# Kernel optimization log

Measured on AMD Instinct MI355X. Metric: run time of the kernel, lower is better.

## Reference

```python
import jax, jax.numpy as jnp
import numpy as np

B, T, DH, DS, A = 32, 2048, 1024, 1024, 512

def setup_inputs() -> dict:
    key = jax.random.key(0)
    k1, k2, k3, k4, k5 = jax.random.split(key, 5)
    s = jax.random.normal(k1, (B, DS), dtype=jnp.float32)
    h = jax.random.normal(k2, (B, T, DH), dtype=jnp.float32)
    # glorot_uniform for W_a, U_a; uniform(-0.05, 0.05) for v_a (Keras defaults)
    lim_W = np.sqrt(6.0 / (DS + A)).astype(np.float32)
    lim_U = np.sqrt(6.0 / (DH + A)).astype(np.float32)
    W_a = jax.random.uniform(k3, (DS, A), minval=-lim_W, maxval=lim_W, dtype=jnp.float32)
    U_a = jax.random.uniform(k4, (DH, A), minval=-lim_U, maxval=lim_U, dtype=jnp.float32)
    v_a = jax.random.uniform(k5, (A,), minval=-0.05, maxval=0.05, dtype=jnp.float32)
    return {"s": s, "h": h, "W_a": W_a, "U_a": U_a, "v_a": v_a}

def reference(s, h, W_a, U_a, v_a):
    # U_a_h: [B, T, A]; W_a_s: [B, 1, A]
    U_a_h = jnp.einsum('btd,da->bta', h, U_a)
    W_a_s = (s @ W_a)[:, None, :]
    e = jnp.tanh(W_a_s + U_a_h)          # [B, T, A]
    e = jnp.einsum('bta,a->bt', e, v_a)   # learned-vector reduction
    a = jax.nn.softmax(e, axis=-1)        # exp / sum over time (same math, stable)
    c = jnp.einsum('bt,btd->bd', a, h)    # weighted sum over time
    return c
```

## Files before the change

kernel.cpp:

```cpp
#include <hip/hip_runtime.h>
#include <hip/hip_bf16.h>

#define B_  32
#define T_  2048
#define DH_ 1024
#define DS_ 1024
#define A_  512
#define M_  (B_ * T_)

typedef __attribute__((ext_vector_type(8))) short bf16x8;
typedef __attribute__((ext_vector_type(4))) float f32x4;

__device__ __forceinline__ unsigned short f2bf(float f) {
    union { float f; unsigned u; } v; v.f = f;
    unsigned r = 0x7FFFu + ((v.u >> 16) & 1u);
    return (unsigned short)((v.u + r) >> 16);
}
__device__ __forceinline__ float fast_tanh(float x) {
    float cx = fminf(fmaxf(x, -9.f), 9.f);
    float e2 = __expf(2.f * cx);
    return (e2 - 1.f) / (e2 + 1.f);
}
__device__ __forceinline__ unsigned pack_bf2(float lo, float hi) {
    union { float f; unsigned u; } a, b;
    a.f = lo; b.f = hi;
    return __builtin_amdgcn_perm(b.u + 0x8000u, a.u + 0x8000u, 0x07060302u);
}

__global__ void prep_ut(const float* __restrict__ U, unsigned short* __restrict__ Ut) {
    int o = blockIdx.x * 256 + threadIdx.x;
    int a = o >> 10, k = o & (DH_ - 1);
    Ut[o] = f2bf(U[k * A_ + a]);
}

__global__ void ws_gemv2(const float* __restrict__ s, const float* __restrict__ W,
                         float* __restrict__ Ws) {
    __shared__ float red[4][64];
    const int blk = blockIdx.x;
    const int b = blk >> 3, a0 = (blk & 7) * 64;
    const int tid = threadIdx.x;
    const int a = a0 + (tid & 63), kq = tid >> 6;
    const float* sp = s + b * DS_ + kq * 256;
    const float* wp = W + (size_t)(kq * 256) * A_ + a;
    float acc = 0.f;
#pragma unroll 8
    for (int k = 0; k < 256; ++k) acc += sp[k] * wp[(size_t)k * A_];
    red[kq][tid & 63] = acc;
    __syncthreads();
    if (tid < 64)
        Ws[b * A_ + a0 + tid] = red[0][tid] + red[1][tid] + red[2][tid] + red[3][tid];
}

__global__ void __launch_bounds__(512, 2)
gemm_bn512(const float* __restrict__ h,
           const unsigned short* __restrict__ Ut,
           const float* __restrict__ Ws, const float* __restrict__ va,
           float* __restrict__ e) {
    __shared__ unsigned short As[2][128][32];
    __shared__ unsigned short Bs[2][512][32];

    const int tid = threadIdx.x;
    const int tm = blockIdx.x;
    const int rowBase = tm * 128;

    const int lane = tid & 63;
    const int wid = tid >> 6;
    const int wm = wid >> 2, wn = wid & 3;
    const int lr = lane & 15, kg = lane >> 4;
    const int gsw16 = (kg ^ ((lr >> 1) & 3)) * 8;

    const int ar = tid >> 2;
    const int alg = tid & 3;

    f32x4 acc[4][8];
#pragma unroll
    for (int i = 0; i < 4; ++i)
#pragma unroll
        for (int j = 0; j < 8; ++j) acc[i][j] = (f32x4){0.f, 0.f, 0.f, 0.f};

    auto loadA = [&](float4* areg, int t) {
        const float* hp = h + (size_t)(rowBase + ar) * DH_ + t * 32 + alg * 8;
        areg[0] = *(const float4*)(hp);
        areg[1] = *(const float4*)(hp + 4);
    };
    auto stageB = [&](int buf, int t) {
        const int k0 = t * 32;
#pragma unroll
        for (int j = 0; j < 4; ++j) {
            int byt = j * 8192 + tid * 16;
            int r = byt >> 6;
            int g = ((byt >> 4) & 3) ^ ((r >> 1) & 3);
            const unsigned short* gb = Ut + (size_t)r * DH_ + k0 + g * 8;
            __builtin_amdgcn_global_load_lds(
                (const __attribute__((address_space(1))) unsigned int*)gb,
                (__attribute__((address_space(3))) unsigned int*)(&Bs[buf][0][0] + (byt >> 1)),
                16, 0, 0);
        }
    };
    auto packwriteA = [&](const float4* areg, int buf) {
        uint4 u;
        u.x = pack_bf2(areg[0].x, areg[0].y);
        u.y = pack_bf2(areg[0].z, areg[0].w);
        u.z = pack_bf2(areg[1].x, areg[1].y);
        u.w = pack_bf2(areg[1].z, areg[1].w);
        int p = alg ^ ((ar >> 1) & 3);
        *(uint4*)((char*)&As[buf][0][0] + ar * 64 + p * 16) = u;
    };

    float4 areg[2];
    const int NT = DH_ / 32;

    loadA(areg, 0);
    __builtin_amdgcn_sched_barrier(0);
    stageB(0, 0);
    __builtin_amdgcn_sched_barrier(0);
    packwriteA(areg, 0);
    asm volatile("s_waitcnt vmcnt(0) lgkmcnt(0)" ::: "memory");
    __builtin_amdgcn_s_barrier();
    __builtin_amdgcn_sched_barrier(0);

#pragma unroll 1
    for (int t = 0; t < NT; ++t) {
        const int buf = t & 1;
        const bool more = (t < NT - 1);
        if (more) {
            loadA(areg, t + 1);
            __builtin_amdgcn_sched_barrier(0);
            stageB(buf ^ 1, t + 1);
            __builtin_amdgcn_sched_barrier(0);
        }

        const unsigned short* Ab = &As[buf][0][0];
        const unsigned short* Bb = &Bs[buf][0][0];
        bf16x8 af[4], bq[8];
#pragma unroll
        for (int nf = 0; nf < 8; ++nf)
            bq[nf] = *(const bf16x8*)(Bb + (wn * 128 + nf * 16 + lr) * 32 + gsw16);
#pragma unroll
        for (int mi = 0; mi < 4; ++mi)
            af[mi] = *(const bf16x8*)(Ab + (wm * 64 + mi * 16 + lr) * 32 + gsw16);
        asm volatile("s_waitcnt lgkmcnt(0)" ::: "memory");
        __builtin_amdgcn_sched_barrier(0);

        __builtin_amdgcn_s_setprio(1);
#pragma unroll
        for (int mi = 0; mi < 4; ++mi)
#pragma unroll
            for (int nf = 0; nf < 8; ++nf)
                acc[mi][nf] = __builtin_amdgcn_mfma_f32_16x16x32_bf16(
                    af[mi], bq[nf], acc[mi][nf], 0, 0, 0);
        __builtin_amdgcn_s_setprio(0);
        __builtin_amdgcn_sched_barrier(0);

        if (more) {
            packwriteA(areg, buf ^ 1);
            asm volatile("s_waitcnt vmcnt(0) lgkmcnt(0)" ::: "memory");
            __builtin_amdgcn_s_barrier();
            __builtin_amdgcn_sched_barrier(0);
        }
    }
    __syncthreads();

    const int bIdx = rowBase >> 11;
    const float* WsRow = Ws + bIdx * A_;
    float wsv[8], vav[8];
#pragma unroll
    for (int nf = 0; nf < 8; ++nf) {
        int a = wn * 128 + nf * 16 + lr;
        wsv[nf] = WsRow[a];
        vav[nf] = va[a];
    }
    float* pf = (float*)&As[0][0][0];
#pragma unroll
    for (int mi = 0; mi < 4; ++mi) {
#pragma unroll
        for (int j = 0; j < 4; ++j) {
            float ssum = 0.f;
#pragma unroll
            for (int nf = 0; nf < 8; ++nf) {
                float x = acc[mi][nf][j] + wsv[nf];
                ssum += fast_tanh(x) * vav[nf];
            }
            ssum += __shfl_xor(ssum, 1);
            ssum += __shfl_xor(ssum, 2);
            ssum += __shfl_xor(ssum, 4);
            ssum += __shfl_xor(ssum, 8);
            if (lr == 0) {
                int r = wm * 64 + mi * 16 + kg * 4 + j;
                pf[r * 4 + wn] = ssum;
            }
        }
    }
    __syncthreads();
    if (tid < 128) {
        float v0 = pf[tid * 4 + 0] + pf[tid * 4 + 1] + pf[tid * 4 + 2] + pf[tid * 4 + 3];
        e[rowBase + tid] = v0;
    }
}

__global__ void smax_ctx(const float* __restrict__ e, const float* __restrict__ h,
                         float* __restrict__ c) {
    __shared__ float al[T_];
    __shared__ float red[8];
    __shared__ float part[256];
    const int b = blockIdx.x >> 3, dseg = blockIdx.x & 7;
    const int tid = threadIdx.x;
    const float* ep = e + (size_t)b * T_;

    float4 v0 = ((const float4*)ep)[tid * 2];
    float4 v1 = ((const float4*)ep)[tid * 2 + 1];
    float m = fmaxf(fmaxf(fmaxf(v0.x, v0.y), fmaxf(v0.z, v0.w)),
                    fmaxf(fmaxf(v1.x, v1.y), fmaxf(v1.z, v1.w)));
#pragma unroll
    for (int off = 1; off < 64; off <<= 1) m = fmaxf(m, __shfl_xor(m, off));
    const int wv = tid >> 6;
    if ((tid & 63) == 0) red[wv] = m;
    __syncthreads();
    m = fmaxf(fmaxf(red[0], red[1]), fmaxf(red[2], red[3]));
    float e0 = __expf(v0.x - m), e1 = __expf(v0.y - m);
    float e2 = __expf(v0.z - m), e3 = __expf(v0.w - m);
    float e4 = __expf(v1.x - m), e5 = __expf(v1.y - m);
    float e6 = __expf(v1.z - m), e7 = __expf(v1.w - m);
    float ssum = e0 + e1 + e2 + e3 + e4 + e5 + e6 + e7;
#pragma unroll
    for (int off = 1; off < 64; off <<= 1) ssum += __shfl_xor(ssum, off);
    if ((tid & 63) == 0) red[4 + wv] = ssum;
    al[tid * 8 + 0] = e0; al[tid * 8 + 1] = e1;
    al[tid * 8 + 2] = e2; al[tid * 8 + 3] = e3;
    al[tid * 8 + 4] = e4; al[tid * 8 + 5] = e5;
    al[tid * 8 + 6] = e6; al[tid * 8 + 7] = e7;
    __syncthreads();
    const float inv = 1.f / (red[4] + red[5] + red[6] + red[7]);

    const int d = dseg * 128 + (tid & 127);
    const int th = tid >> 7;
    const float* hp = h + ((size_t)b * T_ + th) * DH_ + d;
    float acc = 0.f;
#pragma unroll 8
    for (int t = 0; t < T_ / 2; ++t)
        acc += al[2 * t + th] * hp[(size_t)(2 * t) * DH_];
    part[tid] = acc;
    __syncthreads();
    if (tid < 128)
        c[(size_t)b * DH_ + dseg * 128 + tid] = (part[tid] + part[tid + 128]) * inv;
}

extern "C" void kernel_launch(void* const* d_in, const int* in_sizes, int n_in,
                              void* d_out, int out_size, void* d_ws, size_t ws_size,
                              hipStream_t stream) {
    const float* s   = (const float*)d_in[0];
    const float* h   = (const float*)d_in[1];
    const float* W_a = (const float*)d_in[2];
    const float* U_a = (const float*)d_in[3];
    const float* v_a = (const float*)d_in[4];
    float* c = (float*)d_out;

    float* e  = (float*)d_ws;
    float* Ws = e + M_;
    unsigned short* Ut = (unsigned short*)(Ws + B_ * A_);

    prep_ut<<<(A_ * DH_) / 256, 256, 0, stream>>>(U_a, Ut);
    ws_gemv2<<<B_ * 8, 256, 0, stream>>>(s, W_a, Ws);
    gemm_bn512<<<M_ / 128, 512, 0, stream>>>(h, Ut, Ws, v_a, e);
    smax_ctx<<<B_ * 8, 256, 0, stream>>>(e, h, c);
}
```

Baseline: 205.0 us.

## Fuse softmax and context sum into GEMM epilogue with split-T chunk combine

The score GEMM kernel now also computes, for each 128-row time chunk, a local max, the exp weights and their sum, then re-reads the chunk's h rows (likely still in L2) to form a partial context vector. A small combine kernel rescales the 16 chunk partials per batch into the final output, flash-attention style. This removes the separate softmax/context kernel's second full pass over h from HBM. The cost is a serialized tree reduction with many barriers in the epilogue and extra partial-context traffic. The NCH=16 constant assumes 128-row tiles over T=2048.

```diff
diff --git a/kernel.cpp b/kernel.cpp
--- a/kernel.cpp
+++ b/kernel.cpp
@@ -7,6 +7,7 @@
 #define DS_ 1024
 #define A_  512
 #define M_  (B_ * T_)
+#define NCH 16
 
 typedef __attribute__((ext_vector_type(8))) short bf16x8;
 typedef __attribute__((ext_vector_type(4))) float f32x4;
@@ -52,10 +53,11 @@
 }
 
 __global__ void __launch_bounds__(512, 2)
-gemm_bn512(const float* __restrict__ h,
-           const unsigned short* __restrict__ Ut,
-           const float* __restrict__ Ws, const float* __restrict__ va,
-           float* __restrict__ e) {
+fused_chunk(const float* __restrict__ h,
+            const unsigned short* __restrict__ Ut,
+            const float* __restrict__ Ws, const float* __restrict__ va,
+            float* __restrict__ pm, float* __restrict__ pl,
+            float* __restrict__ pc) {
     __shared__ unsigned short As[2][128][32];
     __shared__ unsigned short Bs[2][512][32];
 
@@ -161,6 +163,11 @@
     }
     __syncthreads();
 
+    float* er_s  = (float*)&As[0][0][0];
+    float* red_s = er_s + 128;
+    float* w_s   = er_s + 256;
+    float* pf    = er_s + 384;
+
     const int bIdx = rowBase >> 11;
     const float* WsRow = Ws + bIdx * A_;
     float wsv[8], vav[8];
@@ -170,7 +177,6 @@
         wsv[nf] = WsRow[a];
         vav[nf] = va[a];
     }
-    float* pf = (float*)&As[0][0][0];
 #pragma unroll
     for (int mi = 0; mi < 4; ++mi) {
 #pragma unroll
@@ -193,56 +199,87 @@
     }
     __syncthreads();
     if (tid < 128) {
-        float v0 = pf[tid * 4 + 0] + pf[tid * 4 + 1] + pf[tid * 4 + 2] + pf[tid * 4 + 3];
-        e[rowBase + tid] = v0;
-    }
-}
-
-__global__ void smax_ctx(const float* __restrict__ e, const float* __restrict__ h,
-                         float* __restrict__ c) {
-    __shared__ float al[T_];
-    __shared__ float red[8];
-    __shared__ float part[256];
-    const int b = blockIdx.x >> 3, dseg = blockIdx.x & 7;
+        float v = pf[tid * 4] + pf[tid * 4 + 1] + pf[tid * 4 + 2] + pf[tid * 4 + 3];
+        er_s[tid] = v;
+        red_s[tid] = v;
+    }
+    __syncthreads();
+    if (tid < 64) red_s[tid] = fmaxf(red_s[tid], red_s[tid + 64]);
+    __syncthreads();
+    if (tid < 32) red_s[tid] = fmaxf(red_s[tid], red_s[tid + 32]);
+    __syncthreads();
+    if (tid < 16) red_s[tid] = fmaxf(red_s[tid], red_s[tid + 16]);
+    __syncthreads();
+    if (tid < 8) red_s[tid] = fmaxf(red_s[tid], red_s[tid + 8]);
+    __syncthreads();
+    if (tid < 4) red_s[tid] = fmaxf(red_s[tid], red_s[tid + 4]);
+    __syncthreads();
+    if (tid < 2) red_s[tid] = fmaxf(red_s[tid], red_s[tid + 2]);
+    __syncthreads();
+    if (tid == 0) red_s[0] = fmaxf(red_s[0], red_s[1]);
+    __syncthreads();
+    const float mloc = red_s[0];
+    __syncthreads();
+    if (tid < 128) {
+        float w = __expf(er_s[tid] - mloc);
+        w_s[tid] = w;
+        red_s[tid] = w;
+    }
+    __syncthreads();
+    if (tid < 64) red_s[tid] += red_s[tid + 64];
+    __syncthreads();
+    if (tid < 32) red_s[tid] += red_s[tid + 32];
+    __syncthreads();
+    if (tid < 16) red_s[tid] += red_s[tid + 16];
+    __syncthreads();
+    if (tid < 8) red_s[tid] += red_s[tid + 8];
+    __syncthreads();
+    if (tid < 4) red_s[tid] += red_s[tid + 4];
+    __syncthreads();
+    if (tid < 2) red_s[tid] += red_s[tid + 2];
+    __syncthreads();
+    if (tid == 0) {
+        pm[tm] = mloc;
+        pl[tm] = red_s[0] + red_s[1];
+    }
+
+    float c0 = 0.f, c1 = 0.f;
+    const float* hp = h + (size_t)rowBase * DH_ + tid;
+#pragma unroll 4
+    for (int t = 0; t < 128; ++t) {
+        float w = w_s[t];
+        c0 += w * hp[(size_t)t * DH_];
+        c1 += w * hp[(size_t)t * DH_ + 512];
+    }
+    float* pcp = pc + (size_t)tm * DH_;
+    pcp[tid] = c0;
+    pcp[tid + 512] = c1;
+}
+
+__global__ void combine(const float* __restrict__ pm, const float* __restrict__ pl,
+                        const float* __restrict__ pc, float* __restrict__ c) {
+    const int b = blockIdx.x;
     const int tid = threadIdx.x;
-    const float* ep = e + (size_t)b * T_;
-
-    float4 v0 = ((const float4*)ep)[tid * 2];
-    float4 v1 = ((const float4*)ep)[tid * 2 + 1];
-    float m = fmaxf(fmaxf(fmaxf(v0.x, v0.y), fmaxf(v0.z, v0.w)),
-                    fmaxf(fmaxf(v1.x, v1.y), fmaxf(v1.z, v1.w)));
-#pragma unroll
-    for (int off = 1; off < 64; off <<= 1) m = fmaxf(m, __shfl_xor(m, off));
-    const int wv = tid >> 6;
-    if ((tid & 63) == 0) red[wv] = m;
-    __syncthreads();
-    m = fmaxf(fmaxf(red[0], red[1]), fmaxf(red[2], red[3]));
-    float e0 = __expf(v0.x - m), e1 = __expf(v0.y - m);
-    float e2 = __expf(v0.z - m), e3 = __expf(v0.w - m);
-    float e4 = __expf(v1.x - m), e5 = __expf(v1.y - m);
-    float e6 = __expf(v1.z - m), e7 = __expf(v1.w - m);
-    float ssum = e0 + e1 + e2 + e3 + e4 + e5 + e6 + e7;
-#pragma unroll
-    for (int off = 1; off < 64; off <<= 1) ssum += __shfl_xor(ssum, off);
-    if ((tid & 63) == 0) red[4 + wv] = ssum;
-    al[tid * 8 + 0] = e0; al[tid * 8 + 1] = e1;
-    al[tid * 8 + 2] = e2; al[tid * 8 + 3] = e3;
-    al[tid * 8 + 4] = e4; al[tid * 8 + 5] = e5;
-    al[tid * 8 + 6] = e6; al[tid * 8 + 7] = e7;
-    __syncthreads();
-    const float inv = 1.f / (red[4] + red[5] + red[6] + red[7]);
-
-    const int d = dseg * 128 + (tid & 127);
-    const int th = tid >> 7;
-    const float* hp = h + ((size_t)b * T_ + th) * DH_ + d;
-    float acc = 0.f;
-#pragma unroll 8
-    for (int t = 0; t < T_ / 2; ++t)
-        acc += al[2 * t + th] * hp[(size_t)(2 * t) * DH_];
-    part[tid] = acc;
-    __syncthreads();
-    if (tid < 128)
-        c[(size_t)b * DH_ + dseg * 128 + tid] = (part[tid] + part[tid + 128]) * inv;
+    float M = -1e30f;
+#pragma unroll
+    for (int i = 0; i < NCH; ++i) M = fmaxf(M, pm[b * NCH + i]);
+    float L = 0.f;
+    float sc[NCH];
+#pragma unroll
+    for (int i = 0; i < NCH; ++i) {
+        sc[i] = __expf(pm[b * NCH + i] - M);
+        L += sc[i] * pl[b * NCH + i];
+    }
+    float a0 = 0.f, a1 = 0.f;
+#pragma unroll
+    for (int i = 0; i < NCH; ++i) {
+        const float* pcp = pc + (size_t)(b * NCH + i) * DH_;
+        a0 += sc[i] * pcp[tid];
+        a1 += sc[i] * pcp[tid + 512];
+    }
+    const float inv = 1.f / L;
+    c[(size_t)b * DH_ + tid] = a0 * inv;
+    c[(size_t)b * DH_ + tid + 512] = a1 * inv;
 }
 
 extern "C" void kernel_launch(void* const* d_in, const int* in_sizes, int n_in,
@@ -255,12 +292,14 @@
     const float* v_a = (const float*)d_in[4];
     float* c = (float*)d_out;
 
-    float* e  = (float*)d_ws;
-    float* Ws = e + M_;
+    float* Ws = (float*)d_ws;
     unsigned short* Ut = (unsigned short*)(Ws + B_ * A_);
+    float* pm = (float*)(Ut + (size_t)A_ * DH_);
+    float* pl = pm + B_ * NCH;
+    float* pc = pl + B_ * NCH;
 
     prep_ut<<<(A_ * DH_) / 256, 256, 0, stream>>>(U_a, Ut);
     ws_gemv2<<<B_ * 8, 256, 0, stream>>>(s, W_a, Ws);
-    gemm_bn512<<<M_ / 128, 512, 0, stream>>>(h, Ut, Ws, v_a, e);
-    smax_ctx<<<B_ * 8, 256, 0, stream>>>(e, h, c);
-}
+    fused_chunk<<<B_ * NCH, 512, 0, stream>>>(h, Ut, Ws, v_a, pm, pl, pc);
+    combine<<<B_, 512, 0, stream>>>(pm, pl, pc, c);
+}
```

Measured after the change: 180.6 us, median of 2. -11.9%, faster.
